# Optimization experiments

Measured on AMD Instinct MI355X. Metric: run time of the kernel, lower is better.

## Reference

```python
import jax, jax.numpy as jnp
import numpy as np

B, L, SIZE, ATT, LIN = 8, 2048, 1024, 1024, 4096
EPS = 1e-5


def layer_norm(x, g, b):
    m = x.mean(-1, keepdims=True)
    v = ((x - m) ** 2).mean(-1, keepdims=True)
    return (x - m) * jax.lax.rsqrt(v + EPS) * g + b


def time_shift(x):
    # ZeroPad2d((0,0,1,-1)): prepend a zero timestep, drop the last one
    return jnp.pad(x, ((0, 0), (1, 0), (0, 0)))[:, :-1]


def wkv(time_decay, time_first, k, v):
    """RWKV-v4 WKV linear-attention recurrence (numerically stable, log-space max tracking).
    k, v: (B, L, D). Returns (B, L, D)."""
    w = -jnp.exp(time_decay)  # (D,) per-channel decay (negative)
    u = time_first            # (D,) bonus for current token

    def step(carry, kv):
        p, q, o = carry  # numerator, denominator, running max exponent: (B, D)
        kt, vt = kv      # (B, D)
        no = jnp.maximum(o, u + kt)
        A = jnp.exp(o - no)
        Bc = jnp.exp(u + kt - no)
        out = (A * p + Bc * vt) / (A * q + Bc)
        no2 = jnp.maximum(o + w, kt)
        A2 = jnp.exp(o + w - no2)
        B2 = jnp.exp(kt - no2)
        return (A2 * p + B2 * vt, A2 * q + B2, no2), out

    Bn, Ln, D = k.shape
    init = (jnp.zeros((Bn, D), k.dtype), jnp.zeros((Bn, D), k.dtype),
            jnp.full((Bn, D), -1e38, k.dtype))
    _, out = jax.lax.scan(step, init, (jnp.moveaxis(k, 1, 0), jnp.moveaxis(v, 1, 0)))
    return jnp.moveaxis(out, 0, 1)


def setup_inputs() -> dict:
    key = jax.random.key(0)
    ks = jax.random.split(key, 20)
    n = lambda i, shape, s=1.0: jax.random.normal(ks[i], shape, jnp.float32) * s
    u = lambda i, shape: jax.random.uniform(ks[i], shape, jnp.float32)
    return {
        "x": n(0, (B, L, SIZE)),
        "ln_att_g": jnp.ones((SIZE,), jnp.float32), "ln_att_b": jnp.zeros((SIZE,), jnp.float32),
        "ln_ffn_g": jnp.ones((SIZE,), jnp.float32), "ln_ffn_b": jnp.zeros((SIZE,), jnp.float32),
        "att_time_decay": n(1, (ATT,), 0.5), "att_time_first": n(2, (ATT,), 0.5),
        "att_mix_k": u(3, (SIZE,)), "att_mix_v": u(4, (SIZE,)), "att_mix_r": u(5, (SIZE,)),
        "att_wk": n(6, (SIZE, ATT), 0.02), "att_wv": n(7, (SIZE, ATT), 0.02),
        "att_wr": n(8, (SIZE, ATT), 0.02), "att_wo": n(9, (ATT, SIZE), 0.02),
        "ffn_mix_k": u(10, (SIZE,)), "ffn_mix_r": u(11, (SIZE,)),
        "ffn_wk": n(12, (SIZE, LIN), 0.02), "ffn_wv": n(13, (LIN, SIZE), 0.02),
        "ffn_wr": n(14, (SIZE, SIZE), 0.02),
    }


def reference(x, ln_att_g, ln_att_b, ln_ffn_g, ln_ffn_b,
              att_time_decay, att_time_first, att_mix_k, att_mix_v, att_mix_r,
              att_wk, att_wv, att_wr, att_wo,
              ffn_mix_k, ffn_mix_r, ffn_wk, ffn_wv, ffn_wr):
    # --- time-mixing (WKV attention) branch ---
    h = layer_norm(x, ln_att_g, ln_att_b)
    sx = time_shift(h)
    k = (h * att_mix_k + sx * (1.0 - att_mix_k)) @ att_wk
    v = (h * att_mix_v + sx * (1.0 - att_mix_v)) @ att_wv
    r = jax.nn.sigmoid((h * att_mix_r + sx * (1.0 - att_mix_r)) @ att_wr)
    att = (r * wkv(att_time_decay, att_time_first, k, v)) @ att_wo
    x = x + att  # dropout rate 0.0 (eval)
    # --- channel-mixing (FFN) branch ---
    h = layer_norm(x, ln_ffn_g, ln_ffn_b)
    sx = time_shift(h)
    kf = jnp.square(jax.nn.relu((h * ffn_mix_k + sx * (1.0 - ffn_mix_k)) @ ffn_wk))
    rf = jax.nn.sigmoid((h * ffn_mix_r + sx * (1.0 - ffn_mix_r)) @ ffn_wr)
    return x + rf * (kf @ ffn_wv)
```

## Files before the change

kernel.cpp:

```cpp
#include <hip/hip_runtime.h>
#include <cstdint>
#include <cstddef>

#define BB   8
#define LLEN 2048
#define DSZ  1024
#define FFN  4096
#define MROWS (BB*LLEN)
#define EPSLN 1e-5f
#define WKV_C 32
#define WKV_S (LLEN/WKV_C)
#define WKV_STATES (BB*WKV_C*DSZ)

typedef __bf16 bh8 __attribute__((ext_vector_type(8)));
typedef float  f32x4 __attribute__((ext_vector_type(4)));

__device__ __forceinline__ unsigned short f32_to_bf16(float f) {
  unsigned int u = __float_as_uint(f);
  u += 0x7FFFu + ((u >> 16) & 1u);
  return (unsigned short)(u >> 16);
}
__device__ __forceinline__ float bf16_to_f32(unsigned short u) {
  return __uint_as_float(((unsigned int)u) << 16);
}

__device__ __forceinline__ void load_lds16(const void* g, void* l) {
  __builtin_amdgcn_global_load_lds((const __attribute__((address_space(1))) void*)g,
                                   (__attribute__((address_space(3))) void*)l, 16, 0, 0);
}

#define RAW_BAR() asm volatile("s_barrier" ::: "memory")
#define WAIT_VM6() asm volatile("s_waitcnt vmcnt(6)" ::: "memory")
#define WAIT_VM0() asm volatile("s_waitcnt vmcnt(0)" ::: "memory")
#define WAIT_LGKM0() asm volatile("s_waitcnt lgkmcnt(0)" ::: "memory")

__global__ __launch_bounds__(256) void transpose_bf16(const float* __restrict__ W,
                                                      unsigned short* __restrict__ Wt,
                                                      int K, int N) {
  __shared__ float tile[32][33];
  int n0 = blockIdx.x * 32, k0 = blockIdx.y * 32;
  int tx = threadIdx.x, ty = threadIdx.y;
#pragma unroll
  for (int j = 0; j < 32; j += 8)
    tile[ty + j][tx] = W[(size_t)(k0 + ty + j) * N + n0 + tx];
  __syncthreads();
#pragma unroll
  for (int j = 0; j < 32; j += 8)
    Wt[(size_t)(n0 + ty + j) * K + k0 + tx] = f32_to_bf16(tile[tx][ty + j]);
}

__global__ __launch_bounds__(256) void lnmix_att(const float* __restrict__ x,
                                                 const float* __restrict__ g,
                                                 const float* __restrict__ bb,
                                                 const float* __restrict__ mk,
                                                 const float* __restrict__ mv,
                                                 const float* __restrict__ mr,
                                                 unsigned short* __restrict__ xk,
                                                 unsigned short* __restrict__ xv,
                                                 unsigned short* __restrict__ xr) {
  int row = blockIdx.x;
  int t = row & (LLEN - 1);
  int tid = threadIdx.x;
  float4 vc = ((const float4*)(x + (size_t)row * DSZ))[tid];
  float4 vp = make_float4(0.f, 0.f, 0.f, 0.f);
  if (t > 0) vp = ((const float4*)(x + (size_t)(row - 1) * DSZ))[tid];
  float sc = vc.x + vc.y + vc.z + vc.w;
  float qc = vc.x * vc.x + vc.y * vc.y + vc.z * vc.z + vc.w * vc.w;
  float sp = vp.x + vp.y + vp.z + vp.w;
  float qp = vp.x * vp.x + vp.y * vp.y + vp.z * vp.z + vp.w * vp.w;
#pragma unroll
  for (int off = 32; off; off >>= 1) {
    sc += __shfl_down(sc, off); qc += __shfl_down(qc, off);
    sp += __shfl_down(sp, off); qp += __shfl_down(qp, off);
  }
  __shared__ float red[16];
  int lane = tid & 63, w = tid >> 6;
  if (lane == 0) { red[w] = sc; red[4 + w] = qc; red[8 + w] = sp; red[12 + w] = qp; }
  __syncthreads();
  if (tid < 4) red[tid * 4] = red[tid * 4] + red[tid * 4 + 1] + red[tid * 4 + 2] + red[tid * 4 + 3];
  __syncthreads();
  const float invD = 1.f / DSZ;
  float mc = red[0] * invD, rc = rsqrtf(red[4] * invD - mc * mc + EPSLN);
  float mp = red[8] * invD, rp = rsqrtf(red[12] * invD - mp * mp + EPSLN);
  float4 G = ((const float4*)g)[tid], Bv = ((const float4*)bb)[tid];
  float c[4] = { vc.x, vc.y, vc.z, vc.w };
  float p[4] = { vp.x, vp.y, vp.z, vp.w };
  float Ga[4] = { G.x, G.y, G.z, G.w };
  float Ba[4] = { Bv.x, Bv.y, Bv.z, Bv.w };
  float4 K = ((const float4*)mk)[tid];
  float4 V = ((const float4*)mv)[tid];
  float4 R = ((const float4*)mr)[tid];
  float Ka[4] = { K.x, K.y, K.z, K.w };
  float Va[4] = { V.x, V.y, V.z, V.w };
  float Ra[4] = { R.x, R.y, R.z, R.w };
  ushort4 ok, ov, orr;
  unsigned short* okp = &ok.x; unsigned short* ovp = &ov.x; unsigned short* orp = &orr.x;
#pragma unroll
  for (int e = 0; e < 4; ++e) {
    float hc = (c[e] - mc) * rc * Ga[e] + Ba[e];
    float hp = (t > 0) ? (p[e] - mp) * rp * Ga[e] + Ba[e] : 0.f;
    okp[e] = f32_to_bf16(hc * Ka[e] + hp * (1.f - Ka[e]));
    ovp[e] = f32_to_bf16(hc * Va[e] + hp * (1.f - Va[e]));
    orp[e] = f32_to_bf16(hc * Ra[e] + hp * (1.f - Ra[e]));
  }
  size_t e4 = (size_t)row * DSZ + tid * 4;
  *(ushort4*)(xk + e4) = ok;
  *(ushort4*)(xv + e4) = ov;
  *(ushort4*)(xr + e4) = orr;
}

__global__ __launch_bounds__(256) void lnmix_ffn(const float* __restrict__ x,
                                                 const float* __restrict__ g,
                                                 const float* __restrict__ bb,
                                                 const float* __restrict__ mk,
                                                 const float* __restrict__ mr,
                                                 unsigned short* __restrict__ xk,
                                                 unsigned short* __restrict__ xr) {
  int row = blockIdx.x;
  int t = row & (LLEN - 1);
  int tid = threadIdx.x;
  float4 vc = ((const float4*)(x + (size_t)row * DSZ))[tid];
  float4 vp = make_float4(0.f, 0.f, 0.f, 0.f);
  if (t > 0) vp = ((const float4*)(x + (size_t)(row - 1) * DSZ))[tid];
  float sc = vc.x + vc.y + vc.z + vc.w;
  float qc = vc.x * vc.x + vc.y * vc.y + vc.z * vc.z + vc.w * vc.w;
  float sp = vp.x + vp.y + vp.z + vp.w;
  float qp = vp.x * vp.x + vp.y * vp.y + vp.z * vp.z + vp.w * vp.w;
#pragma unroll
  for (int off = 32; off; off >>= 1) {
    sc += __shfl_down(sc, off); qc += __shfl_down(qc, off);
    sp += __shfl_down(sp, off); qp += __shfl_down(qp, off);
  }
  __shared__ float red[16];
  int lane = tid & 63, w = tid >> 6;
  if (lane == 0) { red[w] = sc; red[4 + w] = qc; red[8 + w] = sp; red[12 + w] = qp; }
  __syncthreads();
  if (tid < 4) red[tid * 4] = red[tid * 4] + red[tid * 4 + 1] + red[tid * 4 + 2] + red[tid * 4 + 3];
  __syncthreads();
  const float invD = 1.f / DSZ;
  float mc = red[0] * invD, rc = rsqrtf(red[4] * invD - mc * mc + EPSLN);
  float mp = red[8] * invD, rp = rsqrtf(red[12] * invD - mp * mp + EPSLN);
  float4 G = ((const float4*)g)[tid], Bv = ((const float4*)bb)[tid];
  float c[4] = { vc.x, vc.y, vc.z, vc.w };
  float p[4] = { vp.x, vp.y, vp.z, vp.w };
  float Ga[4] = { G.x, G.y, G.z, G.w };
  float Ba[4] = { Bv.x, Bv.y, Bv.z, Bv.w };
  float4 K = ((const float4*)mk)[tid];
  float4 R = ((const float4*)mr)[tid];
  float Ka[4] = { K.x, K.y, K.z, K.w };
  float Ra[4] = { R.x, R.y, R.z, R.w };
  ushort4 ok, orr;
  unsigned short* okp = &ok.x; unsigned short* orp = &orr.x;
#pragma unroll
  for (int e = 0; e < 4; ++e) {
    float hc = (c[e] - mc) * rc * Ga[e] + Ba[e];
    float hp = (t > 0) ? (p[e] - mp) * rp * Ga[e] + Ba[e] : 0.f;
    okp[e] = f32_to_bf16(hc * Ka[e] + hp * (1.f - Ka[e]));
    orp[e] = f32_to_bf16(hc * Ra[e] + hp * (1.f - Ra[e]));
  }
  size_t e4 = (size_t)row * DSZ + tid * 4;
  *(ushort4*)(xk + e4) = ok;
  *(ushort4*)(xr + e4) = orr;
}

__global__ __launch_bounds__(256) void wkv_pass1(const unsigned short* __restrict__ kk,
                                                 const unsigned short* __restrict__ vv,
                                                 const float* __restrict__ td,
                                                 float* __restrict__ sP,
                                                 float* __restrict__ sQ,
                                                 float* __restrict__ sO) {
  int gid = blockIdx.x * 256 + threadIdx.x;
  int d  = gid & (DSZ - 1);
  int bc = gid >> 10;
  int c  = bc & (WKV_C - 1);
  int b  = bc >> 5;
  float w = -expf(td[d]);
  size_t base = ((size_t)b * LLEN + (size_t)c * WKV_S) * DSZ + d;
  float p = 0.f, q = 0.f, o = -1e38f;
  float kt = bf16_to_f32(kk[base]);
  float vt = bf16_to_f32(vv[base]);
  for (int t = 0; t < WKV_S; ++t) {
    float kn = 0.f, vn = 0.f;
    if (t < WKV_S - 1) {
      size_t nxt = base + ((size_t)(t + 1) << 10);
      kn = bf16_to_f32(kk[nxt]); vn = bf16_to_f32(vv[nxt]);
    }
    float ow  = o + w;
    float no2 = fmaxf(ow, kt);
    float A2  = expf(ow - no2);
    float B2  = expf(kt - no2);
    p = A2 * p + B2 * vt;
    q = A2 * q + B2;
    o = no2;
    kt = kn; vt = vn;
  }
  sP[gid] = p; sQ[gid] = q; sO[gid] = o;
}

__global__ __launch_bounds__(256) void wkv_combine(const float* __restrict__ sP,
                                                   const float* __restrict__ sQ,
                                                   const float* __restrict__ sO,
                                                   const float* __restrict__ td,
                                                   float* __restrict__ pP,
                                                   float* __restrict__ pQ,
                                                   float* __restrict__ pO) {
  int gid = blockIdx.x * 256 + threadIdx.x;
  int d = gid & (DSZ - 1);
  int b = gid >> 10;
  float w = -expf(td[d]);
  float Sw = (float)WKV_S * w;
  float p = 0.f, q = 0.f, o = -1e38f;
  for (int c = 0; c < WKV_C; ++c) {
    size_t idx = (((size_t)b * WKV_C + c) << 10) + d;
    pP[idx] = p; pQ[idx] = q; pO[idx] = o;
    float lp = sP[idx], lq = sQ[idx], lo = sO[idx];
    float oin = o + Sw;
    float no  = fmaxf(oin, lo);
    float Ai  = expf(oin - no);
    float Al  = expf(lo - no);
    p = Ai * p + Al * lp;
    q = Ai * q + Al * lq;
    o = no;
  }
}

__global__ __launch_bounds__(256) void wkv_pass3(const unsigned short* __restrict__ kk,
                                                 const unsigned short* __restrict__ vv,
                                                 const unsigned short* __restrict__ rr,
                                                 const float* __restrict__ td,
                                                 const float* __restrict__ tf,
                                                 const float* __restrict__ pP,
                                                 const float* __restrict__ pQ,
                                                 const float* __restrict__ pO,
                                                 unsigned short* __restrict__ rw) {
  int gid = blockIdx.x * 256 + threadIdx.x;
  int d  = gid & (DSZ - 1);
  int bc = gid >> 10;
  int c  = bc & (WKV_C - 1);
  int b  = bc >> 5;
  float w = -expf(td[d]);
  float u = tf[d];
  float p = pP[gid], q = pQ[gid], o = pO[gid];
  size_t base = ((size_t)b * LLEN + (size_t)c * WKV_S) * DSZ + d;
  float kt = bf16_to_f32(kk[base]);
  float vt = bf16_to_f32(vv[base]);
  float rt = bf16_to_f32(rr[base]);
  for (int t = 0; t < WKV_S; ++t) {
    float kn = 0.f, vn = 0.f, rn = 0.f;
    if (t < WKV_S - 1) {
      size_t nxt = base + ((size_t)(t + 1) << 10);
      kn = bf16_to_f32(kk[nxt]); vn = bf16_to_f32(vv[nxt]); rn = bf16_to_f32(rr[nxt]);
    }
    float uk = u + kt;
    float no = fmaxf(o, uk);
    float A  = expf(o - no);
    float Bc = expf(uk - no);
    float out = (A * p + Bc * vt) / (A * q + Bc);
    rw[base + ((size_t)t << 10)] = f32_to_bf16(rt * out);
    float ow  = o + w;
    float no2 = fmaxf(ow, kt);
    float A2  = expf(ow - no2);
    float B2  = expf(kt - no2);
    p = A2 * p + B2 * vt;
    q = A2 * q + B2;
    o = no2;
    kt = kn; vt = vn; rt = rn;
  }
}


__device__ __forceinline__ void stage_half(const unsigned short* __restrict__ gsrc,
                                           int Kd, unsigned char* lds_base,
                                           int lane, int wid) {
  int gcol = (((lane & 7) ^ (lane >> 3)) << 3);
  int grow = lane >> 3;
#pragma unroll
  for (int j = 0; j < 2; ++j) {
    int win = wid * 2 + j;
    const unsigned short* src = gsrc + (size_t)(win * 8 + grow) * Kd + gcol;
    load_lds16(src, lds_base + win * 1024 + lane * 16);
  }
}

template <int EPI>
__global__ __launch_bounds__(512, 2) void gemm256(const unsigned short* __restrict__ A,
                                                  const unsigned short* __restrict__ Bt,
                                                  float* __restrict__ C,
                                                  unsigned short* __restrict__ Cbf,
                                                  const float* __restrict__ aux1,
                                                  const unsigned short* __restrict__ aux2b,
                                                  int M, int N, int K) {
  extern __shared__ unsigned char sm[];
  unsigned char* smA = sm;
  unsigned char* smB = sm + 65536;

  const int tid  = threadIdx.x;
  const int lane = tid & 63;
  const int wid  = tid >> 6;
  const int wr   = wid >> 2;
  const int wc   = wid & 3;

  int nwg = gridDim.x;
  int gx  = N >> 8;
  int wg  = blockIdx.x;
  int swzid = ((nwg & 7) == 0) ? ((wg & 7) * (nwg >> 3) + (wg >> 3)) : wg;
  int bn = swzid % gx, bm = swzid / gx;

  const unsigned short* Ab = A  + (size_t)bm * 256 * K;
  const unsigned short* Bb = Bt + (size_t)bn * 256 * K;

  const int nk = K >> 6;

  const int r15 = lane & 15;
  const int sw0 = ((((lane >> 4)    ) ^ (lane & 7)) << 4);
  const int sw1 = (((4 | (lane >> 4)) ^ (lane & 7)) << 4);
  const int aRow = wr * 16384 + r15 * 128;
  const int bRow = wc * 8192  + r15 * 128;

  f32x4 acc[8][4];
#pragma unroll
  for (int i = 0; i < 8; ++i)
#pragma unroll
    for (int j = 0; j < 4; ++j)
#pragma unroll
      for (int e = 0; e < 4; ++e) acc[i][j][e] = 0.f;

  stage_half(Ab,                 K, smA,                 lane, wid);
  stage_half(Ab + (size_t)128*K, K, smA + 16384,         lane, wid);
  stage_half(Bb,                 K, smB,                 lane, wid);
  stage_half(Bb + (size_t)128*K, K, smB + 16384,         lane, wid);
  if (nk > 1) {
    stage_half(Ab + 64,                 K, smA + 32768,         lane, wid);
    stage_half(Ab + (size_t)128*K + 64, K, smA + 32768 + 16384, lane, wid);
    stage_half(Bb + 64,                 K, smB + 32768,         lane, wid);
  }
  WAIT_VM6();
  RAW_BAR();

  for (int t = 0; t < nk; ++t) {
    const int buf  = (t & 1) * 32768;
    const int bufn = ((t + 1) & 1) * 32768;
    const int kb1  = (t + 1) << 6;
    const int kb2  = (t + 2) << 6;

    bh8 a[8][2], b[4][2];
#pragma unroll
    for (int mi = 0; mi < 8; ++mi) {
      a[mi][0] = *(const bh8*)(smA + buf + aRow + mi * 2048 + sw0);
      a[mi][1] = *(const bh8*)(smA + buf + aRow + mi * 2048 + sw1);
    }
#pragma unroll
    for (int nj = 0; nj < 4; ++nj) {
      b[nj][0] = *(const bh8*)(smB + buf + bRow + nj * 2048 + sw0);
      b[nj][1] = *(const bh8*)(smB + buf + bRow + nj * 2048 + sw1);
    }
    if (t + 1 < nk)
      stage_half(Bb + (size_t)128*K + kb1, K, smB + bufn + 16384, lane, wid);
    RAW_BAR();
    __builtin_amdgcn_s_setprio(1);
#pragma unroll
    for (int mi = 0; mi < 4; ++mi)
#pragma unroll
      for (int nj = 0; nj < 2; ++nj) {
        acc[mi][nj] = __builtin_amdgcn_mfma_f32_16x16x32_bf16(a[mi][0], b[nj][0], acc[mi][nj], 0, 0, 0);
        acc[mi][nj] = __builtin_amdgcn_mfma_f32_16x16x32_bf16(a[mi][1], b[nj][1], acc[mi][nj], 0, 0, 0);
      }
    __builtin_amdgcn_s_setprio(0);
    WAIT_LGKM0();
    RAW_BAR();

    if (t + 2 < nk) stage_half(Ab + kb2, K, smA + buf, lane, wid);
    RAW_BAR();
    __builtin_amdgcn_s_setprio(1);
#pragma unroll
    for (int mi = 0; mi < 4; ++mi)
#pragma unroll
      for (int nj = 2; nj < 4; ++nj) {
        acc[mi][nj] = __builtin_amdgcn_mfma_f32_16x16x32_bf16(a[mi][0], b[nj][0], acc[mi][nj], 0, 0, 0);
        acc[mi][nj] = __builtin_amdgcn_mfma_f32_16x16x32_bf16(a[mi][1], b[nj][1], acc[mi][nj], 0, 0, 0);
      }
    __builtin_amdgcn_s_setprio(0);
    RAW_BAR();

    if (t + 2 < nk) stage_half(Ab + (size_t)128*K + kb2, K, smA + buf + 16384, lane, wid);
    RAW_BAR();
    __builtin_amdgcn_s_setprio(1);
#pragma unroll
    for (int mi = 4; mi < 8; ++mi)
#pragma unroll
      for (int nj = 0; nj < 2; ++nj) {
        acc[mi][nj] = __builtin_amdgcn_mfma_f32_16x16x32_bf16(a[mi][0], b[nj][0], acc[mi][nj], 0, 0, 0);
        acc[mi][nj] = __builtin_amdgcn_mfma_f32_16x16x32_bf16(a[mi][1], b[nj][1], acc[mi][nj], 0, 0, 0);
      }
    __builtin_amdgcn_s_setprio(0);
    RAW_BAR();

    if (t + 2 < nk) stage_half(Bb + kb2, K, smB + buf, lane, wid);
    RAW_BAR();
    __builtin_amdgcn_s_setprio(1);
#pragma unroll
    for (int mi = 4; mi < 8; ++mi)
#pragma unroll
      for (int nj = 2; nj < 4; ++nj) {
        acc[mi][nj] = __builtin_amdgcn_mfma_f32_16x16x32_bf16(a[mi][0], b[nj][0], acc[mi][nj], 0, 0, 0);
        acc[mi][nj] = __builtin_amdgcn_mfma_f32_16x16x32_bf16(a[mi][1], b[nj][1], acc[mi][nj], 0, 0, 0);
      }
    __builtin_amdgcn_s_setprio(0);
    if (t + 2 < nk) { WAIT_VM6(); } else { WAIT_VM0(); }
    RAW_BAR();
  }

  const int r4 = (lane >> 4) * 4, cn = lane & 15;
#pragma unroll
  for (int mi = 0; mi < 8; ++mi) {
#pragma unroll
    for (int nj = 0; nj < 4; ++nj) {
      int col = bn * 256 + wc * 64 + nj * 16 + cn;
#pragma unroll
      for (int e = 0; e < 4; ++e) {
        int row = bm * 256 + wr * 128 + mi * 16 + r4 + e;
        size_t idx = (size_t)row * N + col;
        float val = acc[mi][nj][e];
        if (EPI == 0) {
          Cbf[idx] = f32_to_bf16(val);
        } else if (EPI == 1) {
          Cbf[idx] = f32_to_bf16(1.f / (1.f + expf(-val)));
        } else if (EPI == 2) {
          C[idx] = aux1[idx] + val;
        } else if (EPI == 3) {
          float tt = val > 0.f ? val : 0.f;
          Cbf[idx] = f32_to_bf16(tt * tt);
        } else {
          C[idx] = aux1[idx] + bf16_to_f32(aux2b[idx]) * val;
        }
      }
    }
  }
}

extern "C" void kernel_launch(void* const* d_in, const int* in_sizes, int n_in,
                              void* d_out, int out_size, void* d_ws, size_t ws_size,
                              hipStream_t stream) {
  const float* x        = (const float*)d_in[0];
  const float* ln_att_g = (const float*)d_in[1];
  const float* ln_att_b = (const float*)d_in[2];
  const float* ln_ffn_g = (const float*)d_in[3];
  const float* ln_ffn_b = (const float*)d_in[4];
  const float* td       = (const float*)d_in[5];
  const float* tf       = (const float*)d_in[6];
  const float* amk      = (const float*)d_in[7];
  const float* amv      = (const float*)d_in[8];
  const float* amr      = (const float*)d_in[9];
  const float* att_wk   = (const float*)d_in[10];
  const float* att_wv   = (const float*)d_in[11];
  const float* att_wr   = (const float*)d_in[12];
  const float* att_wo   = (const float*)d_in[13];
  const float* fmk      = (const float*)d_in[14];
  const float* fmr      = (const float*)d_in[15];
  const float* ffn_wk   = (const float*)d_in[16];
  const float* ffn_wv   = (const float*)d_in[17];
  const float* ffn_wr   = (const float*)d_in[18];
  float* out = (float*)d_out;
  (void)in_sizes; (void)n_in; (void)out_size;

  const size_t WBYTES  = 4 * ((size_t)DSZ * DSZ * 2)
                       + (size_t)FFN * DSZ * 2
                       + (size_t)DSZ * FFN * 2
                       + (size_t)DSZ * DSZ * 2;
  const size_t BUF     = (size_t)MROWS * DSZ * 2;
  const size_t NEEDED  = WBYTES + 4 * BUF + 2 * BUF;
  if (ws_size < NEEDED) return;

  char* ws = (char*)d_ws;
  size_t off = 0;
  auto take = [&](size_t bytes) { char* p = ws + off; off += (bytes + 255) & ~(size_t)255; return p; };

  unsigned short* wkT  = (unsigned short*)take((size_t)DSZ * DSZ * 2);
  unsigned short* wvT  = (unsigned short*)take((size_t)DSZ * DSZ * 2);
  unsigned short* wrT  = (unsigned short*)take((size_t)DSZ * DSZ * 2);
  unsigned short* woT  = (unsigned short*)take((size_t)DSZ * DSZ * 2);
  unsigned short* fwkT = (unsigned short*)take((size_t)FFN * DSZ * 2);
  unsigned short* fwvT = (unsigned short*)take((size_t)DSZ * FFN * 2);
  unsigned short* fwrT = (unsigned short*)take((size_t)DSZ * DSZ * 2);
  unsigned short* bufA = (unsigned short*)take(BUF);
  unsigned short* bufB = (unsigned short*)take(BUF);
  unsigned short* bufC = (unsigned short*)take(BUF);
  unsigned short* bufD = (unsigned short*)take(BUF);
  char*           eReg = take(2 * BUF);
  unsigned short* kf = bufC;

  float* sP = (float*)eReg;
  float* sQ = sP + WKV_STATES;
  float* sO = sQ + WKV_STATES;
  float* pP = sO + WKV_STATES;
  float* pQ = pP + WKV_STATES;
  float* pO = pQ + WKV_STATES;

  dim3 tb(32, 8);
  transpose_bf16<<<dim3(DSZ / 32, DSZ / 32), tb, 0, stream>>>(att_wk, wkT, DSZ, DSZ);
  transpose_bf16<<<dim3(DSZ / 32, DSZ / 32), tb, 0, stream>>>(att_wv, wvT, DSZ, DSZ);
  transpose_bf16<<<dim3(DSZ / 32, DSZ / 32), tb, 0, stream>>>(att_wr, wrT, DSZ, DSZ);
  transpose_bf16<<<dim3(DSZ / 32, DSZ / 32), tb, 0, stream>>>(att_wo, woT, DSZ, DSZ);
  transpose_bf16<<<dim3(FFN / 32, DSZ / 32), tb, 0, stream>>>(ffn_wk, fwkT, DSZ, FFN);
  transpose_bf16<<<dim3(DSZ / 32, FFN / 32), tb, 0, stream>>>(ffn_wv, fwvT, FFN, DSZ);
  transpose_bf16<<<dim3(DSZ / 32, DSZ / 32), tb, 0, stream>>>(ffn_wr, fwrT, DSZ, DSZ);

  const int LDSB = 131072;
  const int G1   = (MROWS / 256) * (DSZ / 256);
  const int G2   = (MROWS / 256) * (FFN / 256);

  lnmix_att<<<MROWS, 256, 0, stream>>>(x, ln_att_g, ln_att_b, amk, amv, amr, bufA, bufB, bufC);
  gemm256<0><<<G1, 512, LDSB, stream>>>(bufA, wkT, nullptr, bufD, nullptr, nullptr, MROWS, DSZ, DSZ);
  gemm256<0><<<G1, 512, LDSB, stream>>>(bufB, wvT, nullptr, bufA, nullptr, nullptr, MROWS, DSZ, DSZ);
  gemm256<1><<<G1, 512, LDSB, stream>>>(bufC, wrT, nullptr, bufB, nullptr, nullptr, MROWS, DSZ, DSZ);
  wkv_pass1<<<WKV_STATES / 256, 256, 0, stream>>>(bufD, bufA, td, sP, sQ, sO);
  wkv_combine<<<(BB * DSZ) / 256, 256, 0, stream>>>(sP, sQ, sO, td, pP, pQ, pO);
  wkv_pass3<<<WKV_STATES / 256, 256, 0, stream>>>(bufD, bufA, bufB, td, tf, pP, pQ, pO, bufC);
  gemm256<2><<<G1, 512, LDSB, stream>>>(bufC, woT, out, nullptr, x, nullptr, MROWS, DSZ, DSZ);

  lnmix_ffn<<<MROWS, 256, 0, stream>>>(out, ln_ffn_g, ln_ffn_b, fmk, fmr, bufA, bufB);
  gemm256<3><<<G2, 512, LDSB, stream>>>(bufA, fwkT, nullptr, kf, nullptr, nullptr, MROWS, FFN, DSZ);
  gemm256<1><<<G1, 512, LDSB, stream>>>(bufB, fwrT, nullptr, bufA, nullptr, nullptr, MROWS, DSZ, DSZ);
  gemm256<4><<<G1, 512, LDSB, stream>>>(kf, fwvT, out, nullptr, out, bufA, MROWS, DSZ, FFN);
}
```

Before: 697.5 us.

## Vectorize WKV scans over channel pairs and restructure GEMM LDS fragment loading

The WKV pass1 and pass3 kernels now process two adjacent channels per thread. They use 32-bit packed bf16 loads and stores with a two-step-ahead prefetch, which halves the thread count and widens memory accesses. The GEMM main loop now loads A and B fragments from LDS in quarters, interleaved with the MFMA phases, instead of loading all fragments up front. It also reorders the async stage_half refills and drops the explicit lgkmcnt wait. This is meant to lower register pressure and overlap LDS reads with compute, but it relies on the compiler inserting correct LDS waits and on the revised buffer-reuse ordering being race-free.

```diff
diff --git a/kernel.cpp b/kernel.cpp
--- a/kernel.cpp
+++ b/kernel.cpp
@@ -23,6 +23,15 @@
 __device__ __forceinline__ float bf16_to_f32(unsigned short u) {
   return __uint_as_float(((unsigned int)u) << 16);
 }
+__device__ __forceinline__ float bf16_lo(unsigned int u) {
+  return __uint_as_float(u << 16);
+}
+__device__ __forceinline__ float bf16_hi(unsigned int u) {
+  return __uint_as_float(u & 0xFFFF0000u);
+}
+__device__ __forceinline__ unsigned int pack_bf16(float lo, float hi) {
+  return (unsigned int)f32_to_bf16(lo) | ((unsigned int)f32_to_bf16(hi) << 16);
+}
 
 __device__ __forceinline__ void load_lds16(const void* g, void* l) {
   __builtin_amdgcn_global_load_lds((const __attribute__((address_space(1))) void*)g,
@@ -32,7 +41,6 @@
 #define RAW_BAR() asm volatile("s_barrier" ::: "memory")
 #define WAIT_VM6() asm volatile("s_waitcnt vmcnt(6)" ::: "memory")
 #define WAIT_VM0() asm volatile("s_waitcnt vmcnt(0)" ::: "memory")
-#define WAIT_LGKM0() asm volatile("s_waitcnt lgkmcnt(0)" ::: "memory")
 
 __global__ __launch_bounds__(256) void transpose_bf16(const float* __restrict__ W,
                                                       unsigned short* __restrict__ Wt,
@@ -163,38 +171,50 @@
   *(ushort4*)(xr + e4) = orr;
 }
 
-__global__ __launch_bounds__(256) void wkv_pass1(const unsigned short* __restrict__ kk,
-                                                 const unsigned short* __restrict__ vv,
+__global__ __launch_bounds__(256) void wkv_pass1(const unsigned int* __restrict__ kk2,
+                                                 const unsigned int* __restrict__ vv2,
                                                  const float* __restrict__ td,
                                                  float* __restrict__ sP,
                                                  float* __restrict__ sQ,
                                                  float* __restrict__ sO) {
   int gid = blockIdx.x * 256 + threadIdx.x;
-  int d  = gid & (DSZ - 1);
-  int bc = gid >> 10;
+  int d2 = gid & 511;
+  int bc = gid >> 9;
   int c  = bc & (WKV_C - 1);
   int b  = bc >> 5;
-  float w = -expf(td[d]);
-  size_t base = ((size_t)b * LLEN + (size_t)c * WKV_S) * DSZ + d;
-  float p = 0.f, q = 0.f, o = -1e38f;
-  float kt = bf16_to_f32(kk[base]);
-  float vt = bf16_to_f32(vv[base]);
+  int d0 = d2 * 2;
+  float w0 = -expf(td[d0]), w1 = -expf(td[d0 + 1]);
+  size_t base = ((size_t)b * LLEN + (size_t)c * WKV_S) * 512 + d2;
+  float p0 = 0.f, q0 = 0.f, o0 = -1e38f;
+  float p1 = 0.f, q1 = 0.f, o1 = -1e38f;
+  unsigned int kc = kk2[base], vc = vv2[base];
+  unsigned int kA = 0, vA = 0, kB = 0, vB = 0;
+  if (WKV_S > 1) { kA = kk2[base + 512]; vA = vv2[base + 512]; }
   for (int t = 0; t < WKV_S; ++t) {
-    float kn = 0.f, vn = 0.f;
-    if (t < WKV_S - 1) {
-      size_t nxt = base + ((size_t)(t + 1) << 10);
-      kn = bf16_to_f32(kk[nxt]); vn = bf16_to_f32(vv[nxt]);
-    }
-    float ow  = o + w;
-    float no2 = fmaxf(ow, kt);
-    float A2  = expf(ow - no2);
-    float B2  = expf(kt - no2);
-    p = A2 * p + B2 * vt;
-    q = A2 * q + B2;
-    o = no2;
-    kt = kn; vt = vn;
-  }
-  sP[gid] = p; sQ[gid] = q; sO[gid] = o;
+    if (t + 2 < WKV_S) {
+      size_t nxt = base + (size_t)(t + 2) * 512;
+      kB = kk2[nxt]; vB = vv2[nxt];
+    } else { kB = 0; vB = 0; }
+    {
+      float kt = bf16_lo(kc), vt = bf16_lo(vc);
+      float ow = o0 + w0;
+      float no2 = fmaxf(ow, kt);
+      float A2 = expf(ow - no2), B2 = expf(kt - no2);
+      p0 = A2 * p0 + B2 * vt; q0 = A2 * q0 + B2; o0 = no2;
+    }
+    {
+      float kt = bf16_hi(kc), vt = bf16_hi(vc);
+      float ow = o1 + w1;
+      float no2 = fmaxf(ow, kt);
+      float A2 = expf(ow - no2), B2 = expf(kt - no2);
+      p1 = A2 * p1 + B2 * vt; q1 = A2 * q1 + B2; o1 = no2;
+    }
+    kc = kA; vc = vA; kA = kB; vA = vB;
+  }
+  int sidx = (bc << 10) + d0;
+  sP[sidx] = p0; sP[sidx + 1] = p1;
+  sQ[sidx] = q0; sQ[sidx + 1] = q1;
+  sO[sidx] = o0; sO[sidx + 1] = o1;
 }
 
 __global__ __launch_bounds__(256) void wkv_combine(const float* __restrict__ sP,
@@ -224,47 +244,60 @@
   }
 }
 
-__global__ __launch_bounds__(256) void wkv_pass3(const unsigned short* __restrict__ kk,
-                                                 const unsigned short* __restrict__ vv,
-                                                 const unsigned short* __restrict__ rr,
+__global__ __launch_bounds__(256) void wkv_pass3(const unsigned int* __restrict__ kk2,
+                                                 const unsigned int* __restrict__ vv2,
+                                                 const unsigned int* __restrict__ rr2,
                                                  const float* __restrict__ td,
                                                  const float* __restrict__ tf,
                                                  const float* __restrict__ pP,
                                                  const float* __restrict__ pQ,
                                                  const float* __restrict__ pO,
-                                                 unsigned short* __restrict__ rw) {
+                                                 unsigned int* __restrict__ rw2) {
   int gid = blockIdx.x * 256 + threadIdx.x;
-  int d  = gid & (DSZ - 1);
-  int bc = gid >> 10;
+  int d2 = gid & 511;
+  int bc = gid >> 9;
   int c  = bc & (WKV_C - 1);
   int b  = bc >> 5;
-  float w = -expf(td[d]);
-  float u = tf[d];
-  float p = pP[gid], q = pQ[gid], o = pO[gid];
-  size_t base = ((size_t)b * LLEN + (size_t)c * WKV_S) * DSZ + d;
-  float kt = bf16_to_f32(kk[base]);
-  float vt = bf16_to_f32(vv[base]);
-  float rt = bf16_to_f32(rr[base]);
+  int d0 = d2 * 2;
+  float w0 = -expf(td[d0]), w1 = -expf(td[d0 + 1]);
+  float u0 = tf[d0], u1 = tf[d0 + 1];
+  int sidx = (bc << 10) + d0;
+  float p0 = pP[sidx], q0 = pQ[sidx], o0 = pO[sidx];
+  float p1 = pP[sidx + 1], q1 = pQ[sidx + 1], o1 = pO[sidx + 1];
+  size_t base = ((size_t)b * LLEN + (size_t)c * WKV_S) * 512 + d2;
+  unsigned int kc = kk2[base], vc = vv2[base], rc = rr2[base];
+  unsigned int kA = 0, vA = 0, rA = 0, kB = 0, vB = 0, rB = 0;
+  if (WKV_S > 1) { kA = kk2[base + 512]; vA = vv2[base + 512]; rA = rr2[base + 512]; }
   for (int t = 0; t < WKV_S; ++t) {
-    float kn = 0.f, vn = 0.f, rn = 0.f;
-    if (t < WKV_S - 1) {
-      size_t nxt = base + ((size_t)(t + 1) << 10);
-      kn = bf16_to_f32(kk[nxt]); vn = bf16_to_f32(vv[nxt]); rn = bf16_to_f32(rr[nxt]);
-    }
-    float uk = u + kt;
-    float no = fmaxf(o, uk);
-    float A  = expf(o - no);
-    float Bc = expf(uk - no);
-    float out = (A * p + Bc * vt) / (A * q + Bc);
-    rw[base + ((size_t)t << 10)] = f32_to_bf16(rt * out);
-    float ow  = o + w;
-    float no2 = fmaxf(ow, kt);
-    float A2  = expf(ow - no2);
-    float B2  = expf(kt - no2);
-    p = A2 * p + B2 * vt;
-    q = A2 * q + B2;
-    o = no2;
-    kt = kn; vt = vn; rt = rn;
+    if (t + 2 < WKV_S) {
+      size_t nxt = base + (size_t)(t + 2) * 512;
+      kB = kk2[nxt]; vB = vv2[nxt]; rB = rr2[nxt];
+    } else { kB = 0; vB = 0; rB = 0; }
+    float out0, out1;
+    {
+      float kt = bf16_lo(kc), vt = bf16_lo(vc);
+      float uk = u0 + kt;
+      float no = fmaxf(o0, uk);
+      float A  = expf(o0 - no), Bc = expf(uk - no);
+      out0 = (A * p0 + Bc * vt) / (A * q0 + Bc);
+      float ow = o0 + w0;
+      float no2 = fmaxf(ow, kt);
+      float A2 = expf(ow - no2), B2 = expf(kt - no2);
+      p0 = A2 * p0 + B2 * vt; q0 = A2 * q0 + B2; o0 = no2;
+    }
+    {
+      float kt = bf16_hi(kc), vt = bf16_hi(vc);
+      float uk = u1 + kt;
+      float no = fmaxf(o1, uk);
+      float A  = expf(o1 - no), Bc = expf(uk - no);
+      out1 = (A * p1 + Bc * vt) / (A * q1 + Bc);
+      float ow = o1 + w1;
+      float no2 = fmaxf(ow, kt);
+      float A2 = expf(ow - no2), B2 = expf(kt - no2);
+      p1 = A2 * p1 + B2 * vt; q1 = A2 * q1 + B2; o1 = no2;
+    }
+    rw2[base + (size_t)t * 512] = pack_bf16(bf16_lo(rc) * out0, bf16_hi(rc) * out1);
+    kc = kA; vc = vA; rc = rA; kA = kB; vA = vB; rA = rB;
   }
 }
 
@@ -330,29 +363,32 @@
   stage_half(Bb,                 K, smB,                 lane, wid);
   stage_half(Bb + (size_t)128*K, K, smB + 16384,         lane, wid);
   if (nk > 1) {
+    stage_half(Bb + 64,                 K, smB + 32768,         lane, wid);
     stage_half(Ab + 64,                 K, smA + 32768,         lane, wid);
     stage_half(Ab + (size_t)128*K + 64, K, smA + 32768 + 16384, lane, wid);
-    stage_half(Bb + 64,                 K, smB + 32768,         lane, wid);
-  }
-  WAIT_VM6();
+    WAIT_VM6();
+  } else {
+    WAIT_VM0();
+  }
   RAW_BAR();
+
+  bh8 a03[4][2], a47[4][2], b01[2][2], b23[2][2];
 
   for (int t = 0; t < nk; ++t) {
     const int buf  = (t & 1) * 32768;
-    const int bufn = ((t + 1) & 1) * 32768;
+    const int bufn = buf ^ 32768;
     const int kb1  = (t + 1) << 6;
     const int kb2  = (t + 2) << 6;
 
-    bh8 a[8][2], b[4][2];
-#pragma unroll
-    for (int mi = 0; mi < 8; ++mi) {
-      a[mi][0] = *(const bh8*)(smA + buf + aRow + mi * 2048 + sw0);
-      a[mi][1] = *(const bh8*)(smA + buf + aRow + mi * 2048 + sw1);
-    }
-#pragma unroll
-    for (int nj = 0; nj < 4; ++nj) {
-      b[nj][0] = *(const bh8*)(smB + buf + bRow + nj * 2048 + sw0);
-      b[nj][1] = *(const bh8*)(smB + buf + bRow + nj * 2048 + sw1);
+#pragma unroll
+    for (int mi = 0; mi < 4; ++mi) {
+      a03[mi][0] = *(const bh8*)(smA + buf + aRow + mi * 2048 + sw0);
+      a03[mi][1] = *(const bh8*)(smA + buf + aRow + mi * 2048 + sw1);
+    }
+#pragma unroll
+    for (int nj = 0; nj < 2; ++nj) {
+      b01[nj][0] = *(const bh8*)(smB + buf + bRow + nj * 2048 + sw0);
+      b01[nj][1] = *(const bh8*)(smB + buf + bRow + nj * 2048 + sw1);
     }
     if (t + 1 < nk)
       stage_half(Bb + (size_t)128*K + kb1, K, smB + bufn + 16384, lane, wid);
@@ -362,48 +398,59 @@
     for (int mi = 0; mi < 4; ++mi)
 #pragma unroll
       for (int nj = 0; nj < 2; ++nj) {
-        acc[mi][nj] = __builtin_amdgcn_mfma_f32_16x16x32_bf16(a[mi][0], b[nj][0], acc[mi][nj], 0, 0, 0);
-        acc[mi][nj] = __builtin_amdgcn_mfma_f32_16x16x32_bf16(a[mi][1], b[nj][1], acc[mi][nj], 0, 0, 0);
+        acc[mi][nj] = __builtin_amdgcn_mfma_f32_16x16x32_bf16(a03[mi][0], b01[nj][0], acc[mi][nj], 0, 0, 0);
+        acc[mi][nj] = __builtin_amdgcn_mfma_f32_16x16x32_bf16(a03[mi][1], b01[nj][1], acc[mi][nj], 0, 0, 0);
       }
     __builtin_amdgcn_s_setprio(0);
-    WAIT_LGKM0();
-    RAW_BAR();
-
-    if (t + 2 < nk) stage_half(Ab + kb2, K, smA + buf, lane, wid);
+    RAW_BAR();
+
+#pragma unroll
+    for (int nj = 0; nj < 2; ++nj) {
+      b23[nj][0] = *(const bh8*)(smB + buf + bRow + (nj + 2) * 2048 + sw0);
+      b23[nj][1] = *(const bh8*)(smB + buf + bRow + (nj + 2) * 2048 + sw1);
+    }
     RAW_BAR();
     __builtin_amdgcn_s_setprio(1);
 #pragma unroll
     for (int mi = 0; mi < 4; ++mi)
 #pragma unroll
-      for (int nj = 2; nj < 4; ++nj) {
-        acc[mi][nj] = __builtin_amdgcn_mfma_f32_16x16x32_bf16(a[mi][0], b[nj][0], acc[mi][nj], 0, 0, 0);
-        acc[mi][nj] = __builtin_amdgcn_mfma_f32_16x16x32_bf16(a[mi][1], b[nj][1], acc[mi][nj], 0, 0, 0);
+      for (int nj = 0; nj < 2; ++nj) {
+        acc[mi][nj + 2] = __builtin_amdgcn_mfma_f32_16x16x32_bf16(a03[mi][0], b23[nj][0], acc[mi][nj + 2], 0, 0, 0);
+        acc[mi][nj + 2] = __builtin_amdgcn_mfma_f32_16x16x32_bf16(a03[mi][1], b23[nj][1], acc[mi][nj + 2], 0, 0, 0);
       }
     __builtin_amdgcn_s_setprio(0);
     RAW_BAR();
 
-    if (t + 2 < nk) stage_half(Ab + (size_t)128*K + kb2, K, smA + buf + 16384, lane, wid);
+#pragma unroll
+    for (int mi = 0; mi < 4; ++mi) {
+      a47[mi][0] = *(const bh8*)(smA + buf + aRow + (mi + 4) * 2048 + sw0);
+      a47[mi][1] = *(const bh8*)(smA + buf + aRow + (mi + 4) * 2048 + sw1);
+    }
+    if (t + 2 < nk) stage_half(Bb + kb2, K, smB + buf, lane, wid);
     RAW_BAR();
     __builtin_amdgcn_s_setprio(1);
 #pragma unroll
-    for (int mi = 4; mi < 8; ++mi)
+    for (int mi = 0; mi < 4; ++mi)
 #pragma unroll
       for (int nj = 0; nj < 2; ++nj) {
-        acc[mi][nj] = __builtin_amdgcn_mfma_f32_16x16x32_bf16(a[mi][0], b[nj][0], acc[mi][nj], 0, 0, 0);
-        acc[mi][nj] = __builtin_amdgcn_mfma_f32_16x16x32_bf16(a[mi][1], b[nj][1], acc[mi][nj], 0, 0, 0);
+        acc[mi + 4][nj] = __builtin_amdgcn_mfma_f32_16x16x32_bf16(a47[mi][0], b01[nj][0], acc[mi + 4][nj], 0, 0, 0);
+        acc[mi + 4][nj] = __builtin_amdgcn_mfma_f32_16x16x32_bf16(a47[mi][1], b01[nj][1], acc[mi + 4][nj], 0, 0, 0);
       }
     __builtin_amdgcn_s_setprio(0);
     RAW_BAR();
 
-    if (t + 2 < nk) stage_half(Bb + kb2, K, smB + buf, lane, wid);
+    if (t + 2 < nk) {
+      stage_half(Ab + kb2,                 K, smA + buf,         lane, wid);
+      stage_half(Ab + (size_t)128*K + kb2, K, smA + buf + 16384, lane, wid);
+    }
     RAW_BAR();
     __builtin_amdgcn_s_setprio(1);
 #pragma unroll
-    for (int mi = 4; mi < 8; ++mi)
-#pragma unroll
-      for (int nj = 2; nj < 4; ++nj) {
-        acc[mi][nj] = __builtin_amdgcn_mfma_f32_16x16x32_bf16(a[mi][0], b[nj][0], acc[mi][nj], 0, 0, 0);
-        acc[mi][nj] = __builtin_amdgcn_mfma_f32_16x16x32_bf16(a[mi][1], b[nj][1], acc[mi][nj], 0, 0, 0);
+    for (int mi = 0; mi < 4; ++mi)
+#pragma unroll
+      for (int nj = 0; nj < 2; ++nj) {
+        acc[mi + 4][nj + 2] = __builtin_amdgcn_mfma_f32_16x16x32_bf16(a47[mi][0], b23[nj][0], acc[mi + 4][nj + 2], 0, 0, 0);
+        acc[mi + 4][nj + 2] = __builtin_amdgcn_mfma_f32_16x16x32_bf16(a47[mi][1], b23[nj][1], acc[mi + 4][nj + 2], 0, 0, 0);
       }
     __builtin_amdgcn_s_setprio(0);
     if (t + 2 < nk) { WAIT_VM6(); } else { WAIT_VM0(); }
@@ -513,9 +560,9 @@
   gemm256<0><<<G1, 512, LDSB, stream>>>(bufA, wkT, nullptr, bufD, nullptr, nullptr, MROWS, DSZ, DSZ);
   gemm256<0><<<G1, 512, LDSB, stream>>>(bufB, wvT, nullptr, bufA, nullptr, nullptr, MROWS, DSZ, DSZ);
   gemm256<1><<<G1, 512, LDSB, stream>>>(bufC, wrT, nullptr, bufB, nullptr, nullptr, MROWS, DSZ, DSZ);
-  wkv_pass1<<<WKV_STATES / 256, 256, 0, stream>>>(bufD, bufA, td, sP, sQ, sO);
+  wkv_pass1<<<(WKV_STATES / 2) / 256, 256, 0, stream>>>((const unsigned int*)bufD, (const unsigned int*)bufA, td, sP, sQ, sO);
   wkv_combine<<<(BB * DSZ) / 256, 256, 0, stream>>>(sP, sQ, sO, td, pP, pQ, pO);
-  wkv_pass3<<<WKV_STATES / 256, 256, 0, stream>>>(bufD, bufA, bufB, td, tf, pP, pQ, pO, bufC);
+  wkv_pass3<<<(WKV_STATES / 2) / 256, 256, 0, stream>>>((const unsigned int*)bufD, (const unsigned int*)bufA, (const unsigned int*)bufB, td, tf, pP, pQ, pO, (unsigned int*)bufC);
   gemm256<2><<<G1, 512, LDSB, stream>>>(bufC, woT, out, nullptr, x, nullptr, MROWS, DSZ, DSZ);
 
   lnmix_ffn<<<MROWS, 256, 0, stream>>>(out, ln_ffn_g, ln_ffn_b, fmk, fmr, bufA, bufB);
```

Measured after the change: 685.5 us. About the same (-1.7%).
